# Performance work log

Hardware: AMD Instinct MI355X
Metric: run time of the kernel (lower is better)

## Reference

```python
import jax, jax.numpy as jnp
import numpy as np

B, S, E = 4, 4096, 1024
H, D, L = 16, 64, 64   # heads, head_dim, landmarks
KS = 33                # depthwise conv kernel size (seq dim)
N_ITER = 6


def setup_inputs() -> dict:
    key = jax.random.key(0)
    ks = jax.random.split(key, 8)
    s = 0.02
    return {
        "hidden_states": jax.random.normal(ks[0], (B, S, E), dtype=jnp.float32),
        "Wq": jax.random.normal(ks[1], (E, E), dtype=jnp.float32) * s,
        "bq": jnp.zeros((E,), dtype=jnp.float32),
        "Wk": jax.random.normal(ks[2], (E, E), dtype=jnp.float32) * s,
        "bk": jnp.zeros((E,), dtype=jnp.float32),
        "Wv": jax.random.normal(ks[3], (E, E), dtype=jnp.float32) * s,
        "bv": jnp.zeros((E,), dtype=jnp.float32),
        "conv_w": jax.random.normal(ks[4], (H, 1, KS, 1), dtype=jnp.float32) * 0.1,
    }


def _iterative_pinv_original(a, n_iter=N_ITER):
    # a: [B,H,L,L]. Faithful to _pinv_original_nystrom: GLOBAL max over all batches/heads.
    eye = jnp.eye(a.shape[-1], dtype=a.dtype)
    val = a.swapaxes(-1, -2) / jnp.max(jnp.sum(a, axis=-2))
    for _ in range(n_iter):
        kv = a @ val
        val = 0.25 * val @ (13.0 * eye - kv @ (15.0 * eye - kv @ (7.0 * eye - kv)))
    return val


def reference(hidden_states, Wq, bq, Wk, bk, Wv, bv, conv_w):
    scale = D ** -0.25  # divide q and k each by head_dim**0.25

    def heads(x):  # [B,S,E] -> [B,H,S,D]
        return x.reshape(B, S, H, D).transpose(0, 2, 1, 3)

    q = heads(hidden_states @ Wq + bq) * scale
    k = heads(hidden_states @ Wk + bk) * scale
    v = heads(hidden_states @ Wv + bv)

    # landmark means over segments of length S//L
    ql = q.reshape(B, H, L, S // L, D).mean(axis=-2)  # [B,H,L,D]
    kl = k.reshape(B, H, L, S // L, D).mean(axis=-2)  # [B,H,L,D]

    kernel_1 = jax.nn.softmax(jnp.einsum('bhsd,bhld->bhsl', q, kl), axis=-1)   # [B,H,S,L]
    kernel_2 = jax.nn.softmax(jnp.einsum('bhmd,bhld->bhml', ql, kl), axis=-1)  # [B,H,L,L]
    kernel_3 = jax.nn.softmax(jnp.einsum('bhld,bhsd->bhls', ql, k), axis=-1)   # [B,H,L,S]

    pinv = _iterative_pinv_original(kernel_2)
    attention_probs = kernel_1 @ pinv            # [B,H,S,L]
    new_value = kernel_3 @ v                     # [B,H,L,D]
    ctx = attention_probs @ new_value            # [B,H,S,D]

    # depthwise conv skip on value_layer: Conv2d(H,H,(KS,1),groups=H,bias=False)
    pad = KS // 2
    conv_out = jax.lax.conv_general_dilated(
        v, conv_w, window_strides=(1, 1), padding=((pad, pad), (0, 0)),
        dimension_numbers=('NCHW', 'OIHW', 'NCHW'), feature_group_count=H)
    ctx = ctx + conv_out

    return ctx.transpose(0, 2, 1, 3).reshape(B, S, H * D)
```

## Files before the change

kernel.cpp:

```cpp
#include <hip/hip_runtime.h>
#include <stdint.h>

typedef unsigned short u16;
typedef float f32x4 __attribute__((ext_vector_type(4)));
typedef __bf16 bf16x8 __attribute__((ext_vector_type(8)));
typedef u16 u16x8 __attribute__((ext_vector_type(8)));
typedef u16 u16x4 __attribute__((ext_vector_type(4)));

#define SCALE_QK 0.35355339059327373f

#define BAR() asm volatile("s_barrier" ::: "memory")
#define WAIT_LGKM0() do { asm volatile("s_waitcnt lgkmcnt(0)" ::: "memory"); __builtin_amdgcn_sched_barrier(0); } while (0)
#define WAIT_VM(n) do { asm volatile("s_waitcnt vmcnt(" #n ")" ::: "memory"); __builtin_amdgcn_sched_barrier(0); } while (0)

__device__ __forceinline__ u16 f2bf(float f) {
  union { float f; uint32_t u; } x; x.f = f;
  uint32_t r = x.u + 0x7fffu + ((x.u >> 16) & 1u);
  return (u16)(r >> 16);
}
__device__ __forceinline__ float bf2f(u16 h) {
  union { uint32_t u; float f; } x; x.u = ((uint32_t)h) << 16;
  return x.f;
}
__device__ __forceinline__ void gload16(const void* g, void* l) {
  __builtin_amdgcn_global_load_lds((const __attribute__((address_space(1))) void*)g,
                                   (__attribute__((address_space(3))) void*)l, 16, 0, 0);
}
__device__ __forceinline__ bf16x8 ld_f32_to_bf8(const float* p) {
  f32x4 a = *(const f32x4*)p, b = *(const f32x4*)(p + 4);
  union { u16x8 u; bf16x8 h; } c;
  c.u[0] = f2bf(a[0]); c.u[1] = f2bf(a[1]); c.u[2] = f2bf(a[2]); c.u[3] = f2bf(a[3]);
  c.u[4] = f2bf(b[0]); c.u[5] = f2bf(b[1]); c.u[6] = f2bf(b[2]); c.u[7] = f2bf(b[3]);
  return c.h;
}

__global__ __launch_bounds__(256) void k_prep(const float* __restrict__ hidden,
                                              const float* __restrict__ Wq, const float* __restrict__ Wk,
                                              const float* __restrict__ Wv,
                                              u16* __restrict__ hb, u16* __restrict__ Wt) {
  __shared__ float tile[64][65];
  const int bx = blockIdx.x;
  const int t = threadIdx.x;
  if (bx < 8192) {
    const size_t i = ((size_t)bx * 256 + t) * 8;
    f32x4 v0 = *(const f32x4*)(hidden + i);
    f32x4 v1 = *(const f32x4*)(hidden + i + 4);
    u16x8 o;
    o[0] = f2bf(v0[0]); o[1] = f2bf(v0[1]); o[2] = f2bf(v0[2]); o[3] = f2bf(v0[3]);
    o[4] = f2bf(v1[0]); o[5] = f2bf(v1[1]); o[6] = f2bf(v1[2]); o[7] = f2bf(v1[3]);
    *(u16x8*)(hb + i) = o;
    return;
  }
  const int bxx = bx - 8192;
  const int w = bxx >> 8, tn = (bxx >> 4) & 15, tk = bxx & 15;
  const float* W = (w == 0) ? Wq : ((w == 1) ? Wk : Wv);
  const int r = t >> 2, c0 = (t & 3) * 16;
  const float* src = W + (size_t)(tk * 64 + r) * 1024 + tn * 64 + c0;
#pragma unroll
  for (int j = 0; j < 16; j += 4) {
    f32x4 x = *(const f32x4*)(src + j);
    tile[r][c0 + j + 0] = x[0]; tile[r][c0 + j + 1] = x[1];
    tile[r][c0 + j + 2] = x[2]; tile[r][c0 + j + 3] = x[3];
  }
  __syncthreads();
  u16* dst = Wt + (size_t)(w * 1024 + tn * 64 + r) * 1024 + tk * 64 + c0;
#pragma unroll
  for (int j = 0; j < 16; ++j) dst[j] = f2bf(tile[c0 + j][r]);
}

__device__ __forceinline__ bf16x8 frg(const u16* buf, int row, int ks, int lhi) {
  const int ck = (ks << 2) + lhi;
  return *reinterpret_cast<const bf16x8*>(buf + (row << 6) + ((ck ^ (row & 7)) << 3));
}
__device__ __forceinline__ void issue(const u16* g, int rowbase, int tc, u16* ldsbase, int wid) {
  gload16(g + (((size_t)rowbase) << 10) + tc, ldsbase + ((rowbase + (wid << 3)) << 6));
}
template <int Q>
__device__ __forceinline__ void quad_mfma(const bf16x8 (&af)[2][2], const bf16x8 (&bf)[4][2],
                                          f32x4 (&acc)[8][4]) {
#pragma unroll
  for (int mm = 0; mm < 2; ++mm)
#pragma unroll
    for (int n = 0; n < 4; ++n) {
      acc[Q * 2 + mm][n] = __builtin_amdgcn_mfma_f32_16x16x32_bf16(af[mm][0], bf[n][0], acc[Q * 2 + mm][n], 0, 0, 0);
      acc[Q * 2 + mm][n] = __builtin_amdgcn_mfma_f32_16x16x32_bf16(af[mm][1], bf[n][1], acc[Q * 2 + mm][n], 0, 0, 0);
    }
}
#define LOADA_TO(dst, Q)                                     \
  dst[0][0] = frg(ASr, rA0 + (Q)*32, 0, lhi);                \
  dst[0][1] = frg(ASr, rA0 + (Q)*32, 1, lhi);                \
  dst[1][0] = frg(ASr, rA0 + (Q)*32 + 16, 0, lhi);           \
  dst[1][1] = frg(ASr, rA0 + (Q)*32 + 16, 1, lhi);

__global__ __launch_bounds__(512) void k_gemm2(const u16* __restrict__ A, const u16* __restrict__ Bt,
                                               const float* __restrict__ bq, const float* __restrict__ bk,
                                               const float* __restrict__ bv,
                                               u16* __restrict__ oq, u16* __restrict__ ok, u16* __restrict__ ov,
                                               float* __restrict__ ql, float* __restrict__ kl) {
  __shared__ __align__(16) u16 AS[2][256 * 64];
  __shared__ __align__(16) u16 BS[2][256 * 64];
  __shared__ __align__(16) u16 obuf[8][16][70];
  const int t = threadIdx.x, lane = t & 63, wid = t >> 6;
  const int wm = wid >> 2, wn = wid & 3;
  const int bi = blockIdx.x;
  const int bm = ((bi & 7) << 3) + (bi >> 3) / 12;
  const int bn = (bi >> 3) % 12;
  const int l15 = lane & 15, lhi = lane >> 4;

  const int rowoff = t >> 3;
  const int cswz = (t & 7) ^ (rowoff & 7);
  const u16* aG = A + (((size_t)(bm * 256 + rowoff)) << 10) + (cswz << 3);
  const u16* bG = Bt + (((size_t)(bn * 256 + rowoff)) << 10) + (cswz << 3);

  const int rA0 = wm * 128 + l15;
  const int rB0 = wn * 64 + l15;

  f32x4 acc[8][4];
#pragma unroll
  for (int m = 0; m < 8; ++m)
#pragma unroll
    for (int n = 0; n < 4; ++n) acc[m][n] = (f32x4){0.f, 0.f, 0.f, 0.f};

  issue(bG, 0, 0, BS[0], wid);
  issue(bG, 64, 0, BS[0], wid);
  issue(bG, 128, 0, BS[0], wid);
  issue(bG, 192, 0, BS[0], wid);
  issue(aG, 0, 0, AS[0], wid);
  issue(aG, 128, 0, AS[0], wid);
  issue(aG, 64, 0, AS[0], wid);
  issue(aG, 192, 0, AS[0], wid);
  WAIT_VM(2);
  BAR();

  for (int u = 0; u < 15; ++u) {
    const int pu = u & 1;
    const u16* ASr = AS[pu];
    const u16* BSr = BS[pu];
    u16* ASw = AS[pu ^ 1];
    u16* BSw = BS[pu ^ 1];
    const int tc = (u + 1) << 6;
    bf16x8 bfr[4][2];
    bf16x8 afA[2][2], afB[2][2];
#pragma unroll
    for (int n = 0; n < 4; ++n) {
      bfr[n][0] = frg(BSr, rB0 + n * 16, 0, lhi);
      bfr[n][1] = frg(BSr, rB0 + n * 16, 1, lhi);
    }
    LOADA_TO(afA, 0)
    LOADA_TO(afB, 1)
    issue(bG, 0, tc, BSw, wid);
    issue(bG, 64, tc, BSw, wid);
    issue(bG, 128, tc, BSw, wid);
    issue(bG, 192, tc, BSw, wid);
    issue(aG, 0, tc, ASw, wid);
    issue(aG, 128, tc, ASw, wid);
    issue(aG, 64, tc, ASw, wid);
    issue(aG, 192, tc, ASw, wid);
    __builtin_amdgcn_s_setprio(1);
    quad_mfma<0>(afA, bfr, acc);
    __builtin_amdgcn_s_setprio(0);
    WAIT_VM(8);
    BAR();
    LOADA_TO(afA, 2)
    __builtin_amdgcn_s_setprio(1);
    quad_mfma<1>(afB, bfr, acc);
    __builtin_amdgcn_s_setprio(0);
    LOADA_TO(afB, 3)
    __builtin_amdgcn_s_setprio(1);
    quad_mfma<2>(afA, bfr, acc);
    __builtin_amdgcn_s_setprio(0);
    __builtin_amdgcn_s_setprio(1);
    quad_mfma<3>(afB, bfr, acc);
    __builtin_amdgcn_s_setprio(0);
    WAIT_VM(2);
    BAR();
  }
  {
    const u16* ASr = AS[1];
    const u16* BSr = BS[1];
    bf16x8 bfr[4][2];
    bf16x8 afA[2][2], afB[2][2];
#pragma unroll
    for (int n = 0; n < 4; ++n) {
      bfr[n][0] = frg(BSr, rB0 + n * 16, 0, lhi);
      bfr[n][1] = frg(BSr, rB0 + n * 16, 1, lhi);
    }
    LOADA_TO(afA, 0)
    LOADA_TO(afB, 1)
    quad_mfma<0>(afA, bfr, acc);
    WAIT_VM(0);
    BAR();
    LOADA_TO(afA, 2)
    quad_mfma<1>(afB, bfr, acc);
    LOADA_TO(afB, 3)
    quad_mfma<2>(afA, bfr, acc);
    quad_mfma<3>(afB, bfr, acc);
  }

  const int which = bn >> 2;
  const float* bias = (which == 0) ? bq : ((which == 1) ? bk : bv);
  u16* op = (which == 0) ? oq : ((which == 1) ? ok : ov);
  const float scl = (which < 2) ? SCALE_QK : 1.0f;
  const int h = ((bn & 3) << 2) + wn;
  const int rowBase2 = (bm << 8) + (wm << 7);
  const int rl = lhi << 2;
  const int srow = lane >> 2, d0 = (lane & 3) * 16;
  float bb[4];
#pragma unroll
  for (int n = 0; n < 4; ++n) bb[n] = bias[((bn & 3) << 8) + (wn << 6) + n * 16 + l15];
#pragma unroll
  for (int m = 0; m < 8; ++m) {
#pragma unroll
    for (int n = 0; n < 4; ++n)
#pragma unroll
      for (int r = 0; r < 4; ++r)
        obuf[wid][rl + r][n * 16 + l15] = f2bf((acc[m][n][r] + bb[n]) * scl);
    const int gm = rowBase2 + m * 16 + srow;
    const int b_ = gm >> 12, s = gm & 4095;
    u16* dst = op + (((size_t)b_ * 16 + h) * 4096 + s) * 64 + d0;
    *(u16x8*)dst = *(const u16x8*)&obuf[wid][srow][d0];
    *(u16x8*)(dst + 8) = *(const u16x8*)&obuf[wid][srow][d0 + 8];
  }
  if (which < 2) {
    float* lmp = (which == 0) ? ql : kl;
    const int bh = ((bm >> 4) << 4) + h;
#pragma unroll
    for (int sg = 0; sg < 2; ++sg) {
#pragma unroll
      for (int n = 0; n < 4; ++n) {
        float s = 0.f;
#pragma unroll
        for (int mi = 0; mi < 4; ++mi)
#pragma unroll
          for (int r = 0; r < 4; ++r) s += (acc[sg * 4 + mi][n][r] + bb[n]) * scl;
        s += __shfl_xor(s, 16, 64);
        s += __shfl_xor(s, 32, 64);
        if (lhi == 0) {
          const int lseg = ((bm & 15) << 2) + (wm << 1) + sg;
          lmp[(size_t)bh * 4096 + lseg * 64 + n * 16 + l15] = s * 0.015625f;
        }
      }
    }
  }
}

__global__ __launch_bounds__(256) void k_k2(const float* __restrict__ ql, const float* __restrict__ kl,
                                            float* __restrict__ k2t, float* __restrict__ colmax,
                                            u16* __restrict__ klb) {
  __shared__ __align__(16) float qlT[64 * 68];
  __shared__ __align__(16) float klT[64 * 68];
  __shared__ __align__(16) float sc[64 * 68];
  const int bh = blockIdx.x, t = threadIdx.x;
  {
    const int r = t >> 2, c0 = (t & 3) * 16;
    const float* qp = ql + (size_t)bh * 4096 + r * 64 + c0;
    const float* kp = kl + (size_t)bh * 4096 + r * 64 + c0;
    u16* kb_ = klb + (size_t)bh * 4096 + r * 64 + c0;
#pragma unroll
    for (int j = 0; j < 16; ++j) {
      qlT[(c0 + j) * 68 + r] = qp[j];
      const float kv = kp[j];
      klT[(c0 + j) * 68 + r] = kv;
      kb_[j] = f2bf(kv);
    }
  }
  __syncthreads();
  {
    const int mg = (t >> 4) * 4, lg = (t & 15) * 4;
    float acc[4][4];
#pragma unroll
    for (int i = 0; i < 4; ++i)
#pragma unroll
      for (int j = 0; j < 4; ++j) acc[i][j] = 0.f;
    for (int d0 = 0; d0 < 64; ++d0) {
      f32x4 x = *(const f32x4*)&qlT[d0 * 68 + mg];
      f32x4 y = *(const f32x4*)&klT[d0 * 68 + lg];
#pragma unroll
      for (int i = 0; i < 4; ++i)
#pragma unroll
        for (int j = 0; j < 4; ++j) acc[i][j] += x[i] * y[j];
    }
#pragma unroll
    for (int i = 0; i < 4; ++i)
#pragma unroll
      for (int j = 0; j < 4; ++j) sc[(mg + i) * 68 + lg + j] = acc[i][j];
  }
  __syncthreads();
  if (t < 64) {
    float mx = -1e30f;
    for (int l = 0; l < 64; ++l) mx = fmaxf(mx, sc[t * 68 + l]);
    float sum = 0.f;
    for (int l = 0; l < 64; ++l) { float e = __expf(sc[t * 68 + l] - mx); sc[t * 68 + l] = e; sum += e; }
    const float inv = 1.0f / sum;
    for (int l = 0; l < 64; ++l) sc[t * 68 + l] *= inv;
  }
  __syncthreads();
  {
    const int r = t >> 2, c0 = (t & 3) * 16;
    float* ot = k2t + (size_t)bh * 4096 + r * 64 + c0;
#pragma unroll
    for (int j = 0; j < 16; ++j) ot[j] = sc[(c0 + j) * 68 + r];
  }
  if (t < 64) {
    float s = 0.f;
    for (int m = 0; m < 64; ++m) s += sc[m * 68 + t];
    for (int off = 32; off; off >>= 1) s = fmaxf(s, __shfl_down(s, off, 64));
    if (t == 0) colmax[bh] = s;
  }
}

__device__ __forceinline__ int pidx(int row, int c) {
  return (row << 6) + ((((c >> 2) ^ (row & 15)) << 2) | (c & 3));
}
__device__ __forceinline__ void mm64s(const float* __restrict__ X, const float* __restrict__ Y,
                                      int row, int c0, float* __restrict__ acc) {
#pragma unroll
  for (int j = 0; j < 8; ++j) acc[j] = 0.f;
  for (int kc = 0; kc < 16; ++kc) {
    f32x4 xq = *(const f32x4*)&X[pidx(row, kc << 2)];
#pragma unroll
    for (int kk = 0; kk < 4; ++kk) {
      const int k = (kc << 2) + kk;
      f32x4 y0 = *(const f32x4*)&Y[pidx(k, c0)];
      f32x4 y1 = *(const f32x4*)&Y[pidx(k, c0 + 4)];
      const float x = xq[kk];
#pragma unroll
      for (int j = 0; j < 4; ++j) { acc[j] += x * y0[j]; acc[4 + j] += x * y1[j]; }
    }
  }
}

__global__ __launch_bounds__(512) void k_mid(const float* __restrict__ k2t, const float* __restrict__ colmax,
                                             float* __restrict__ pinv,
                                             const float* __restrict__ ql, const u16* __restrict__ kb,
                                             const u16* __restrict__ vb,
                                             float* __restrict__ nvp, float* __restrict__ zp) {
  __shared__ __align__(16) char smem_s[81920];
  __shared__ float gsh;
  const int t = threadIdx.x;
  if (blockIdx.x < 64) {
    float* aS = (float*)smem_s;
    float* vl = aS + 4096;
    float* kv = vl + 4096;
    float* t1 = kv + 4096;
    float* t2 = t1 + 4096;
    const int bh = blockIdx.x;
    const float* aT = k2t + (size_t)bh * 4096;
    if (t < 64) {
      float v = colmax[t];
      for (int off = 32; off; off >>= 1) v = fmaxf(v, __shfl_down(v, off, 64));
      if (t == 0) gsh = v;
    }
    const int row = t >> 3, c0 = (t & 7) << 3;
#pragma unroll
    for (int j = 0; j < 8; ++j) {
      const int i = t * 8 + j;
      aS[pidx(i & 63, i >> 6)] = aT[i];
    }
    __syncthreads();
    const float ginv = 1.0f / gsh;
    {
      f32x4 v0 = *(const f32x4*)(aT + row * 64 + c0);
      f32x4 v1 = *(const f32x4*)(aT + row * 64 + c0 + 4);
      v0 *= ginv; v1 *= ginv;
      *(f32x4*)&vl[pidx(row, c0)] = v0;
      *(f32x4*)&vl[pidx(row, c0 + 4)] = v1;
    }
    __syncthreads();
    float acc[8];
    for (int it = 0; it < 6; ++it) {
      mm64s(aS, vl, row, c0, acc);
#pragma unroll
      for (int j = 0; j < 8; ++j) kv[pidx(row, c0 + j)] = acc[j];
      __syncthreads();
#pragma unroll
      for (int j = 0; j < 8; ++j) {
        const int c = c0 + j;
        t1[pidx(row, c)] = ((row == c) ? 7.0f : 0.0f) - kv[pidx(row, c)];
      }
      __syncthreads();
      mm64s(kv, t1, row, c0, acc);
#pragma unroll
      for (int j = 0; j < 8; ++j) {
        const int c = c0 + j;
        t2[pidx(row, c)] = ((row == c) ? 15.0f : 0.0f) - acc[j];
      }
      __syncthreads();
      mm64s(kv, t2, row, c0, acc);
#pragma unroll
      for (int j = 0; j < 8; ++j) {
        const int c = c0 + j;
        t1[pidx(row, c)] = ((row == c) ? 13.0f : 0.0f) - acc[j];
      }
      __syncthreads();
      mm64s(vl, t1, row, c0, acc);
#pragma unroll
      for (int j = 0; j < 8; ++j) t2[pidx(row, c0 + j)] = 0.25f * acc[j];
      __syncthreads();
#pragma unroll
      for (int j = 0; j < 8; ++j) vl[pidx(row, c0 + j)] = t2[pidx(row, c0 + j)];
      __syncthreads();
    }
    {
      f32x4 o0 = *(const f32x4*)&vl[pidx(row, c0)];
      f32x4 o1 = *(const f32x4*)&vl[pidx(row, c0 + 4)];
      *(f32x4*)(pinv + (size_t)bh * 4096 + row * 64 + c0) = o0;
      *(f32x4*)(pinv + (size_t)bh * 4096 + row * 64 + c0 + 4) = o1;
    }
    return;
  }
  u16* VTs = (u16*)smem_s;
  u16* els = (u16*)(smem_s + 36864);
  const int id = (int)blockIdx.x - 64;
  const int bh = id & 63, scn = id >> 6;
  const int lane = t & 63, w = t >> 6;
  const int wq = w & 3, half = w >> 2;
  const int l15 = lane & 15, kg = (lane >> 4) << 3, rl = (lane >> 4) << 2;
  const float* aRow = ql + (size_t)bh * 4096 + (wq * 16 + l15) * 64 + kg;
  bf16x8 aql[2];
  aql[0] = ld_f32_to_bf8(aRow);
  aql[1] = ld_f32_to_bf8(aRow + 32);
  f32x4 accv[4];
#pragma unroll
  for (int n = 0; n < 4; ++n) accv[n] = (f32x4){0.f, 0.f, 0.f, 0.f};
  float zacc[4] = {0.f, 0.f, 0.f, 0.f};
  const int sBase = scn * 512 + half * 256;
  u16* VT0 = VTs + ((size_t)(0 * 2 + half) * 64) * 72;
  u16* VT1 = VTs + ((size_t)(1 * 2 + half) * 64) * 72;
  u16* elw = els + ((size_t)w * 16) * 72;
  {
    const u16* vp = vb + ((size_t)bh * 4096 + sBase + lane) * 64 + wq * 16;
    u16x8 h0 = *(const u16x8*)vp, h1 = *(const u16x8*)(vp + 8);
#pragma unroll
    for (int j = 0; j < 8; ++j) {
      VT0[(wq * 16 + j) * 72 + lane] = h0[j];
      VT0[(wq * 16 + 8 + j) * 72 + lane] = h1[j];
    }
  }
  __syncthreads();
  for (int sub = 0; sub < 4; ++sub) {
    const int s0 = sBase + sub * 64;
    u16x8 hn0 = {0, 0, 0, 0, 0, 0, 0, 0}, hn1 = {0, 0, 0, 0, 0, 0, 0, 0};
    if (sub < 3) {
      const u16* vpn = vb + ((size_t)bh * 4096 + s0 + 64 + lane) * 64 + wq * 16;
      hn0 = *(const u16x8*)vpn; hn1 = *(const u16x8*)(vpn + 8);
    }
    const u16* bRow = kb + ((size_t)bh * 4096 + s0 + l15) * 64 + kg;
    f32x4 e[4];
#pragma unroll
    for (int n = 0; n < 4; ++n) e[n] = (f32x4){0.f, 0.f, 0.f, 0.f};
#pragma unroll
    for (int ks = 0; ks < 2; ++ks)
#pragma unroll
      for (int n = 0; n < 4; ++n) {
        bf16x8 bk_ = *reinterpret_cast<const bf16x8*>(bRow + n * 1024 + ks * 32);
        e[n] = __builtin_amdgcn_mfma_f32_16x16x32_bf16(aql[ks], bk_, e[n], 0, 0, 0);
      }
#pragma unroll
    for (int n = 0; n < 4; ++n)
#pragma unroll
      for (int r = 0; r < 4; ++r) {
        const float v = __expf(e[n][r]);
        zacc[r] += v;
        elw[(rl + r) * 72 + n * 16 + l15] = f2bf(v);
      }
    if (sub < 3) {
      u16* VTn = ((sub + 1) & 1) ? VT1 : VT0;
#pragma unroll
      for (int j = 0; j < 8; ++j) {
        VTn[(wq * 16 + j) * 72 + lane] = hn0[j];
        VTn[(wq * 16 + 8 + j) * 72 + lane] = hn1[j];
      }
    }
    WAIT_LGKM0();
    const u16* VTc = (sub & 1) ? VT1 : VT0;
#pragma unroll
    for (int ks = 0; ks < 2; ++ks) {
      bf16x8 af = *reinterpret_cast<const bf16x8*>(&elw[l15 * 72 + kg + ks * 32]);
#pragma unroll
      for (int n = 0; n < 4; ++n) {
        bf16x8 bf_ = *reinterpret_cast<const bf16x8*>(&VTc[(n * 16 + l15) * 72 + kg + ks * 32]);
        accv[n] = __builtin_amdgcn_mfma_f32_16x16x32_bf16(af, bf_, accv[n], 0, 0, 0);
      }
    }
    BAR();
  }
  const int p = scn * 2 + half;
#pragma unroll
  for (int r = 0; r < 4; ++r)
#pragma unroll
    for (int n = 0; n < 4; ++n)
      nvp[(((size_t)p * 64 + bh) * 64 + wq * 16 + rl + r) * 64 + n * 16 + l15] = accv[n][r];
#pragma unroll
  for (int r = 0; r < 4; ++r) {
    float s = zacc[r];
    s += __shfl_xor(s, 1, 64); s += __shfl_xor(s, 2, 64);
    s += __shfl_xor(s, 4, 64); s += __shfl_xor(s, 8, 64);
    if (l15 == 0) zp[((size_t)p * 64 + bh) * 64 + wq * 16 + rl + r] = s;
  }
}

__global__ __launch_bounds__(256) void k_pnv(const float* __restrict__ pinv, const float* __restrict__ nvp,
                                             const float* __restrict__ zp, u16* __restrict__ Mtb) {
  __shared__ __align__(16) float XT[64 * 68];
  __shared__ __align__(16) float Y[64 * 68];
  const int bh = blockIdx.x, t = threadIdx.x;
  {
    const int r = t >> 2, c0 = (t & 3) * 16;
    const float* pp = pinv + (size_t)bh * 4096 + r * 64 + c0;
#pragma unroll
    for (int j = 0; j < 16; ++j) XT[(c0 + j) * 68 + r] = pp[j];
    float zs = 0.f;
#pragma unroll
    for (int p = 0; p < 16; ++p) zs += zp[((size_t)p * 64 + bh) * 64 + r];
    const float iz = 1.0f / zs;
#pragma unroll
    for (int j = 0; j < 16; ++j) {
      float s = 0.f;
#pragma unroll
      for (int p = 0; p < 16; ++p) s += nvp[(((size_t)p * 64 + bh) * 64 + r) * 64 + c0 + j];
      Y[r * 68 + c0 + j] = s * iz;
    }
  }
  __syncthreads();
  const int rg = (t >> 4) * 4, cg = (t & 15) * 4;
  float acc[4][4];
#pragma unroll
  for (int i = 0; i < 4; ++i)
#pragma unroll
    for (int j = 0; j < 4; ++j) acc[i][j] = 0.f;
  for (int k = 0; k < 64; ++k) {
    f32x4 x = *(const f32x4*)&XT[k * 68 + rg];
    f32x4 y = *(const f32x4*)&Y[k * 68 + cg];
#pragma unroll
    for (int i = 0; i < 4; ++i)
#pragma unroll
      for (int j = 0; j < 4; ++j) acc[i][j] += x[i] * y[j];
  }
#pragma unroll
  for (int j = 0; j < 4; ++j) {
    u16x4 o = {f2bf(acc[0][j]), f2bf(acc[1][j]), f2bf(acc[2][j]), f2bf(acc[3][j])};
    *(u16x4*)&Mtb[(size_t)bh * 4096 + (cg + j) * 64 + rg] = o;
  }
}

__global__ __launch_bounds__(256) void k_out(const u16* __restrict__ qb, const u16* __restrict__ vb,
                                             const u16* __restrict__ klb, const u16* __restrict__ Mtb,
                                             const float* __restrict__ cw, float* __restrict__ out) {
  __shared__ __align__(16) u16 P_lds[4][16][72];
  __shared__ __align__(16) u16 vtile_t[64][100];
  __shared__ float wsh[33];
  const int bid = blockIdx.x;
  const int bh = bid >> 6, st = bid & 63;
  const int b = bh >> 4, h = bh & 15;
  const int t = threadIdx.x, lane = t & 63, w = t >> 6;
  const int sbase = st * 64;
  const int l15 = lane & 15, kg = (lane >> 4) << 3, rl = (lane >> 4) << 2;

  if (t < 33) wsh[t] = cw[h * 33 + t];
  for (int idx = t; idx < 96 * 8; idx += 256) {
    const int row = idx >> 3, c8 = idx & 7;
    const int sg = sbase + row - 16;
    u16x8 val = {0, 0, 0, 0, 0, 0, 0, 0};
    if (sg >= 0 && sg < 4096) val = *(const u16x8*)(vb + ((size_t)bh * 4096 + sg) * 64 + c8 * 8);
#pragma unroll
    for (int j = 0; j < 8; ++j) vtile_t[c8 * 8 + j][row] = val[j];
  }

  f32x4 c1[4];
#pragma unroll
  for (int n = 0; n < 4; ++n) c1[n] = (f32x4){0.f, 0.f, 0.f, 0.f};
  {
    const u16* aRow = qb + ((size_t)bh * 4096 + sbase + w * 16 + l15) * 64 + kg;
    const u16* kRow = klb + (size_t)bh * 4096 + l15 * 64 + kg;
#pragma unroll
    for (int ks = 0; ks < 2; ++ks) {
      bf16x8 af = *reinterpret_cast<const bf16x8*>(aRow + ks * 32);
#pragma unroll
      for (int n = 0; n < 4; ++n) {
        bf16x8 bf_ = *reinterpret_cast<const bf16x8*>(kRow + n * 1024 + ks * 32);
        c1[n] = __builtin_amdgcn_mfma_f32_16x16x32_bf16(af, bf_, c1[n], 0, 0, 0);
      }
    }
  }
  float invZ[4];
  {
    float z[4] = {0.f, 0.f, 0.f, 0.f};
#pragma unroll
    for (int n = 0; n < 4; ++n)
#pragma unroll
      for (int r = 0; r < 4; ++r) { float v = __expf(c1[n][r]); c1[n][r] = v; z[r] += v; }
#pragma unroll
    for (int r = 0; r < 4; ++r) {
      float s = z[r];
      s += __shfl_xor(s, 1, 64); s += __shfl_xor(s, 2, 64);
      s += __shfl_xor(s, 4, 64); s += __shfl_xor(s, 8, 64);
      invZ[r] = 1.0f / s;
    }
#pragma unroll
    for (int n = 0; n < 4; ++n)
#pragma unroll
      for (int r = 0; r < 4; ++r)
        P_lds[w][rl + r][n * 16 + l15] = f2bf(c1[n][r]);
  }
  __syncthreads();
  f32x4 c2[4];
#pragma unroll
  for (int n = 0; n < 4; ++n) c2[n] = (f32x4){0.f, 0.f, 0.f, 0.f};
  {
    const u16* mRow = Mtb + (size_t)bh * 4096 + l15 * 64 + kg;
#pragma unroll
    for (int ks = 0; ks < 2; ++ks) {
      bf16x8 af = *reinterpret_cast<const bf16x8*>(&P_lds[w][l15][kg + ks * 32]);
#pragma unroll
      for (int n = 0; n < 4; ++n) {
        bf16x8 bf_ = *reinterpret_cast<const bf16x8*>(mRow + n * 1024 + ks * 32);
        c2[n] = __builtin_amdgcn_mfma_f32_16x16x32_bf16(af, bf_, c2[n], 0, 0, 0);
      }
    }
  }
  const int base = w * 16 + rl;
#pragma unroll
  for (int n = 0; n < 4; ++n) {
    const int d = n * 16 + l15;
    float vcol[36];
#pragma unroll
    for (int k8 = 0; k8 < 9; ++k8) {
      u16x4 vq = *(const u16x4*)&vtile_t[d][base + k8 * 4];
      vcol[k8 * 4 + 0] = bf2f(vq[0]); vcol[k8 * 4 + 1] = bf2f(vq[1]);
      vcol[k8 * 4 + 2] = bf2f(vq[2]); vcol[k8 * 4 + 3] = bf2f(vq[3]);
    }
    float cv[4] = {0.f, 0.f, 0.f, 0.f};
#pragma unroll
    for (int jt = 0; jt < 33; ++jt) {
      const float ww = wsh[jt];
#pragma unroll
      for (int r = 0; r < 4; ++r) cv[r] += ww * vcol[r + jt];
    }
#pragma unroll
    for (int r = 0; r < 4; ++r) {
      const int sgl = sbase + base + r;
      out[((size_t)b * 4096 + sgl) * 1024 + h * 64 + d] = c2[n][r] * invZ[r] + cv[r];
    }
  }
}

extern "C" void kernel_launch(void* const* d_in, const int* in_sizes, int n_in,
                              void* d_out, int out_size, void* d_ws, size_t ws_size,
                              hipStream_t stream) {
  const float* hidden = (const float*)d_in[0];
  const float* Wq = (const float*)d_in[1];
  const float* bq = (const float*)d_in[2];
  const float* Wk = (const float*)d_in[3];
  const float* bk = (const float*)d_in[4];
  const float* Wv = (const float*)d_in[5];
  const float* bv = (const float*)d_in[6];
  const float* cw = (const float*)d_in[7];
  float* out = (float*)d_out;

  char* ws = (char*)d_ws;
  u16* qb = (u16*)(ws);
  u16* kb = (u16*)(ws + 33554432ull);
  u16* vb = (u16*)(ws + 67108864ull);
  float* ql = (float*)(ws + 100663296ull);
  float* kl = (float*)(ws + 101711872ull);
  float* k2t = (float*)(ws + 102760448ull);
  float* pinvb = (float*)(ws + 103809024ull);
  u16* Mtb = (u16*)(ws + 104857600ull);
  u16* klb = (u16*)(ws + 105381888ull);
  float* stats = (float*)(ws + 106430464ull);
  u16* wt = (u16*)(ws + 106434560ull);
  u16* hb = (u16*)(ws + 112726016ull);
  float* nvp = (float*)(ws + 112726016ull);
  float* zp = (float*)(ws + 129503232ull);

  k_prep<<<8960, 256, 0, stream>>>(hidden, Wq, Wk, Wv, hb, wt);
  k_gemm2<<<768, 512, 0, stream>>>(hb, wt, bq, bk, bv, qb, kb, vb, ql, kl);
  k_k2<<<64, 256, 0, stream>>>(ql, kl, k2t, stats, klb);
  k_mid<<<576, 512, 0, stream>>>(k2t, stats, pinvb, ql, kb, vb, nvp, zp);
  k_pnv<<<64, 256, 0, stream>>>(pinvb, nvp, zp, Mtb);
  k_out<<<4096, 256, 0, stream>>>(qb, vb, klb, Mtb, cw, out);
  (void)in_sizes; (void)n_in; (void)out_size; (void)ws_size;
}
```

Before: 318.9 us.

## Reschedule GEMM loads, drop block swizzle, split mid kernel into pinv and s3nv

The QKV GEMM main loop now uses a single A-fragment register set with extra barriers and LDS waits interleaved between the four MFMA quarters. The grouped block-index swizzle is replaced by a plain 2D grid, which loses the L2 locality it provided. The fused k_mid kernel, which ran the pinv and kernel3@V work in separate blocks of one launch, is split into two launches: k_pinv, and k_s3nv with 256-thread blocks each covering 512 sequence positions, so k_pnv reduces 8 partials instead of 16. These look like regressions: extra barriers, worse L2 tiling, and the pinv no longer overlapping the s3nv work.

New measurement: 339.6 us. +6.5%, slower.

```diff
diff --git a/kernel.cpp b/kernel.cpp
--- a/kernel.cpp
+++ b/kernel.cpp
@@ -86,11 +86,11 @@
       acc[Q * 2 + mm][n] = __builtin_amdgcn_mfma_f32_16x16x32_bf16(af[mm][1], bf[n][1], acc[Q * 2 + mm][n], 0, 0, 0);
     }
 }
-#define LOADA_TO(dst, Q)                                     \
-  dst[0][0] = frg(ASr, rA0 + (Q)*32, 0, lhi);                \
-  dst[0][1] = frg(ASr, rA0 + (Q)*32, 1, lhi);                \
-  dst[1][0] = frg(ASr, rA0 + (Q)*32 + 16, 0, lhi);           \
-  dst[1][1] = frg(ASr, rA0 + (Q)*32 + 16, 1, lhi);
+#define LOADA(Q)                                             \
+  af[0][0] = frg(ASr, rA0 + (Q)*32, 0, lhi);                 \
+  af[0][1] = frg(ASr, rA0 + (Q)*32, 1, lhi);                 \
+  af[1][0] = frg(ASr, rA0 + (Q)*32 + 16, 0, lhi);            \
+  af[1][1] = frg(ASr, rA0 + (Q)*32 + 16, 1, lhi);
 
 __global__ __launch_bounds__(512) void k_gemm2(const u16* __restrict__ A, const u16* __restrict__ Bt,
                                                const float* __restrict__ bq, const float* __restrict__ bk,
@@ -102,9 +102,7 @@
   __shared__ __align__(16) u16 obuf[8][16][70];
   const int t = threadIdx.x, lane = t & 63, wid = t >> 6;
   const int wm = wid >> 2, wn = wid & 3;
-  const int bi = blockIdx.x;
-  const int bm = ((bi & 7) << 3) + (bi >> 3) / 12;
-  const int bn = (bi >> 3) % 12;
+  const int bm = blockIdx.x, bn = blockIdx.y;
   const int l15 = lane & 15, lhi = lane >> 4;
 
   const int rowoff = t >> 3;
@@ -140,37 +138,47 @@
     u16* BSw = BS[pu ^ 1];
     const int tc = (u + 1) << 6;
     bf16x8 bfr[4][2];
-    bf16x8 afA[2][2], afB[2][2];
+    bf16x8 af[2][2];
 #pragma unroll
     for (int n = 0; n < 4; ++n) {
       bfr[n][0] = frg(BSr, rB0 + n * 16, 0, lhi);
       bfr[n][1] = frg(BSr, rB0 + n * 16, 1, lhi);
     }
-    LOADA_TO(afA, 0)
-    LOADA_TO(afB, 1)
+    LOADA(0)
     issue(bG, 0, tc, BSw, wid);
     issue(bG, 64, tc, BSw, wid);
     issue(bG, 128, tc, BSw, wid);
     issue(bG, 192, tc, BSw, wid);
+    BAR();
+    WAIT_LGKM0();
+    __builtin_amdgcn_s_setprio(1);
+    quad_mfma<0>(af, bfr, acc);
+    __builtin_amdgcn_s_setprio(0);
+    BAR();
+    LOADA(1)
     issue(aG, 0, tc, ASw, wid);
     issue(aG, 128, tc, ASw, wid);
+    BAR();
+    WAIT_LGKM0();
+    __builtin_amdgcn_s_setprio(1);
+    quad_mfma<1>(af, bfr, acc);
+    __builtin_amdgcn_s_setprio(0);
+    WAIT_VM(6);
+    BAR();
+    LOADA(2)
     issue(aG, 64, tc, ASw, wid);
     issue(aG, 192, tc, ASw, wid);
+    BAR();
+    WAIT_LGKM0();
     __builtin_amdgcn_s_setprio(1);
-    quad_mfma<0>(afA, bfr, acc);
+    quad_mfma<2>(af, bfr, acc);
     __builtin_amdgcn_s_setprio(0);
-    WAIT_VM(8);
-    BAR();
-    LOADA_TO(afA, 2)
+    BAR();
+    LOADA(3)
+    BAR();
+    WAIT_LGKM0();
     __builtin_amdgcn_s_setprio(1);
-    quad_mfma<1>(afB, bfr, acc);
-    __builtin_amdgcn_s_setprio(0);
-    LOADA_TO(afB, 3)
-    __builtin_amdgcn_s_setprio(1);
-    quad_mfma<2>(afA, bfr, acc);
-    __builtin_amdgcn_s_setprio(0);
-    __builtin_amdgcn_s_setprio(1);
-    quad_mfma<3>(afB, bfr, acc);
+    quad_mfma<3>(af, bfr, acc);
     __builtin_amdgcn_s_setprio(0);
     WAIT_VM(2);
     BAR();
@@ -179,22 +187,22 @@
     const u16* ASr = AS[1];
     const u16* BSr = BS[1];
     bf16x8 bfr[4][2];
-    bf16x8 afA[2][2], afB[2][2];
+    bf16x8 af[2][2];
 #pragma unroll
     for (int n = 0; n < 4; ++n) {
       bfr[n][0] = frg(BSr, rB0 + n * 16, 0, lhi);
       bfr[n][1] = frg(BSr, rB0 + n * 16, 1, lhi);
     }
-    LOADA_TO(afA, 0)
-    LOADA_TO(afB, 1)
-    quad_mfma<0>(afA, bfr, acc);
+    LOADA(0)
+    quad_mfma<0>(af, bfr, acc);
+    LOADA(1)
+    quad_mfma<1>(af, bfr, acc);
     WAIT_VM(0);
     BAR();
-    LOADA_TO(afA, 2)
-    quad_mfma<1>(afB, bfr, acc);
-    LOADA_TO(afB, 3)
-    quad_mfma<2>(afA, bfr, acc);
-    quad_mfma<3>(afB, bfr, acc);
+    LOADA(2)
+    quad_mfma<2>(af, bfr, acc);
+    LOADA(3)
+    quad_mfma<3>(af, bfr, acc);
   }
 
   const int which = bn >> 2;
@@ -330,93 +338,88 @@
   }
 }
 
-__global__ __launch_bounds__(512) void k_mid(const float* __restrict__ k2t, const float* __restrict__ colmax,
-                                             float* __restrict__ pinv,
-                                             const float* __restrict__ ql, const u16* __restrict__ kb,
-                                             const u16* __restrict__ vb,
-                                             float* __restrict__ nvp, float* __restrict__ zp) {
-  __shared__ __align__(16) char smem_s[81920];
+__global__ __launch_bounds__(512) void k_pinv(const float* __restrict__ k2t, const float* __restrict__ colmax,
+                                              float* __restrict__ pinv) {
+  __shared__ __align__(16) float aS[4096];
+  __shared__ __align__(16) float vl[4096];
+  __shared__ __align__(16) float kv[4096];
+  __shared__ __align__(16) float t1[4096];
+  __shared__ __align__(16) float t2[4096];
   __shared__ float gsh;
-  const int t = threadIdx.x;
-  if (blockIdx.x < 64) {
-    float* aS = (float*)smem_s;
-    float* vl = aS + 4096;
-    float* kv = vl + 4096;
-    float* t1 = kv + 4096;
-    float* t2 = t1 + 4096;
-    const int bh = blockIdx.x;
-    const float* aT = k2t + (size_t)bh * 4096;
-    if (t < 64) {
-      float v = colmax[t];
-      for (int off = 32; off; off >>= 1) v = fmaxf(v, __shfl_down(v, off, 64));
-      if (t == 0) gsh = v;
-    }
-    const int row = t >> 3, c0 = (t & 7) << 3;
+  const int bh = blockIdx.x, t = threadIdx.x;
+  const float* aT = k2t + (size_t)bh * 4096;
+  if (t < 64) {
+    float v = colmax[t];
+    for (int off = 32; off; off >>= 1) v = fmaxf(v, __shfl_down(v, off, 64));
+    if (t == 0) gsh = v;
+  }
+  const int row = t >> 3, c0 = (t & 7) << 3;
+#pragma unroll
+  for (int j = 0; j < 8; ++j) {
+    const int i = t * 8 + j;
+    aS[pidx(i & 63, i >> 6)] = aT[i];
+  }
+  __syncthreads();
+  const float ginv = 1.0f / gsh;
+  {
+    f32x4 v0 = *(const f32x4*)(aT + row * 64 + c0);
+    f32x4 v1 = *(const f32x4*)(aT + row * 64 + c0 + 4);
+    v0 *= ginv; v1 *= ginv;
+    *(f32x4*)&vl[pidx(row, c0)] = v0;
+    *(f32x4*)&vl[pidx(row, c0 + 4)] = v1;
+  }
+  __syncthreads();
+  float acc[8];
+  for (int it = 0; it < 6; ++it) {
+    mm64s(aS, vl, row, c0, acc);
+#pragma unroll
+    for (int j = 0; j < 8; ++j) kv[pidx(row, c0 + j)] = acc[j];
+    __syncthreads();
 #pragma unroll
     for (int j = 0; j < 8; ++j) {
-      const int i = t * 8 + j;
-      aS[pidx(i & 63, i >> 6)] = aT[i];
+      const int c = c0 + j;
+      t1[pidx(row, c)] = ((row == c) ? 7.0f : 0.0f) - kv[pidx(row, c)];
     }
     __syncthreads();
-    const float ginv = 1.0f / gsh;
-    {
-      f32x4 v0 = *(const f32x4*)(aT + row * 64 + c0);
-      f32x4 v1 = *(const f32x4*)(aT + row * 64 + c0 + 4);
-      v0 *= ginv; v1 *= ginv;
-      *(f32x4*)&vl[pidx(row, c0)] = v0;
-      *(f32x4*)&vl[pidx(row, c0 + 4)] = v1;
+    mm64s(kv, t1, row, c0, acc);
+#pragma unroll
+    for (int j = 0; j < 8; ++j) {
+      const int c = c0 + j;
+      t2[pidx(row, c)] = ((row == c) ? 15.0f : 0.0f) - acc[j];
     }
     __syncthreads();
-    float acc[8];
-    for (int it = 0; it < 6; ++it) {
-      mm64s(aS, vl, row, c0, acc);
-#pragma unroll
-      for (int j = 0; j < 8; ++j) kv[pidx(row, c0 + j)] = acc[j];
-      __syncthreads();
-#pragma unroll
-      for (int j = 0; j < 8; ++j) {
-        const int c = c0 + j;
-        t1[pidx(row, c)] = ((row == c) ? 7.0f : 0.0f) - kv[pidx(row, c)];
-      }
-      __syncthreads();
-      mm64s(kv, t1, row, c0, acc);
-#pragma unroll
-      for (int j = 0; j < 8; ++j) {
-        const int c = c0 + j;
-        t2[pidx(row, c)] = ((row == c) ? 15.0f : 0.0f) - acc[j];
-      }
-      __syncthreads();
-      mm64s(kv, t2, row, c0, acc);
-#pragma unroll
-      for (int j = 0; j < 8; ++j) {
-        const int c = c0 + j;
-        t1[pidx(row, c)] = ((row == c) ? 13.0f : 0.0f) - acc[j];
-      }
-      __syncthreads();
-      mm64s(vl, t1, row, c0, acc);
-#pragma unroll
-      for (int j = 0; j < 8; ++j) t2[pidx(row, c0 + j)] = 0.25f * acc[j];
-      __syncthreads();
-#pragma unroll
-      for (int j = 0; j < 8; ++j) vl[pidx(row, c0 + j)] = t2[pidx(row, c0 + j)];
-      __syncthreads();
-    }
-    {
-      f32x4 o0 = *(const f32x4*)&vl[pidx(row, c0)];
-      f32x4 o1 = *(const f32x4*)&vl[pidx(row, c0 + 4)];
-      *(f32x4*)(pinv + (size_t)bh * 4096 + row * 64 + c0) = o0;
-      *(f32x4*)(pinv + (size_t)bh * 4096 + row * 64 + c0 + 4) = o1;
-    }
-    return;
-  }
-  u16* VTs = (u16*)smem_s;
-  u16* els = (u16*)(smem_s + 36864);
-  const int id = (int)blockIdx.x - 64;
-  const int bh = id & 63, scn = id >> 6;
-  const int lane = t & 63, w = t >> 6;
-  const int wq = w & 3, half = w >> 2;
+    mm64s(kv, t2, row, c0, acc);
+#pragma unroll
+    for (int j = 0; j < 8; ++j) {
+      const int c = c0 + j;
+      t1[pidx(row, c)] = ((row == c) ? 13.0f : 0.0f) - acc[j];
+    }
+    __syncthreads();
+    mm64s(vl, t1, row, c0, acc);
+#pragma unroll
+    for (int j = 0; j < 8; ++j) t2[pidx(row, c0 + j)] = 0.25f * acc[j];
+    __syncthreads();
+#pragma unroll
+    for (int j = 0; j < 8; ++j) vl[pidx(row, c0 + j)] = t2[pidx(row, c0 + j)];
+    __syncthreads();
+  }
+  {
+    f32x4 o0 = *(const f32x4*)&vl[pidx(row, c0)];
+    f32x4 o1 = *(const f32x4*)&vl[pidx(row, c0 + 4)];
+    *(f32x4*)(pinv + (size_t)bh * 4096 + row * 64 + c0) = o0;
+    *(f32x4*)(pinv + (size_t)bh * 4096 + row * 64 + c0 + 4) = o1;
+  }
+}
+
+__global__ __launch_bounds__(256) void k_s3nv(const float* __restrict__ ql, const u16* __restrict__ kb,
+                                              const u16* __restrict__ vb,
+                                              float* __restrict__ nvp, float* __restrict__ zp) {
+  __shared__ __align__(16) u16 VT[2][64][72];
+  __shared__ __align__(16) u16 e_lds[4][16][72];
+  const int bh = blockIdx.x, scn = blockIdx.y;
+  const int t = threadIdx.x, lane = t & 63, w = t >> 6;
   const int l15 = lane & 15, kg = (lane >> 4) << 3, rl = (lane >> 4) << 2;
-  const float* aRow = ql + (size_t)bh * 4096 + (wq * 16 + l15) * 64 + kg;
+  const float* aRow = ql + (size_t)bh * 4096 + (w * 16 + l15) * 64 + kg;
   bf16x8 aql[2];
   aql[0] = ld_f32_to_bf8(aRow);
   aql[1] = ld_f32_to_bf8(aRow + 32);
@@ -424,25 +427,19 @@
 #pragma unroll
   for (int n = 0; n < 4; ++n) accv[n] = (f32x4){0.f, 0.f, 0.f, 0.f};
   float zacc[4] = {0.f, 0.f, 0.f, 0.f};
-  const int sBase = scn * 512 + half * 256;
-  u16* VT0 = VTs + ((size_t)(0 * 2 + half) * 64) * 72;
-  u16* VT1 = VTs + ((size_t)(1 * 2 + half) * 64) * 72;
-  u16* elw = els + ((size_t)w * 16) * 72;
-  {
-    const u16* vp = vb + ((size_t)bh * 4096 + sBase + lane) * 64 + wq * 16;
+  const int sBase = scn * 512;
+  {
+    const u16* vp = vb + ((size_t)bh * 4096 + sBase + lane) * 64 + w * 16;
     u16x8 h0 = *(const u16x8*)vp, h1 = *(const u16x8*)(vp + 8);
 #pragma unroll
-    for (int j = 0; j < 8; ++j) {
-      VT0[(wq * 16 + j) * 72 + lane] = h0[j];
-      VT0[(wq * 16 + 8 + j) * 72 + lane] = h1[j];
-    }
-  }
-  __syncthreads();
-  for (int sub = 0; sub < 4; ++sub) {
+    for (int j = 0; j < 8; ++j) { VT[0][w * 16 + j][lane] = h0[j]; VT[0][w * 16 + 8 + j][lane] = h1[j]; }
+  }
+  __syncthreads();
+  for (int sub = 0; sub < 8; ++sub) {
     const int s0 = sBase + sub * 64;
     u16x8 hn0 = {0, 0, 0, 0, 0, 0, 0, 0}, hn1 = {0, 0, 0, 0, 0, 0, 0, 0};
-    if (sub < 3) {
-      const u16* vpn = vb + ((size_t)bh * 4096 + s0 + 64 + lane) * 64 + wq * 16;
+    if (sub < 7) {
+      const u16* vpn = vb + ((size_t)bh * 4096 + s0 + 64 + lane) * 64 + w * 16;
       hn0 = *(const u16x8*)vpn; hn1 = *(const u16x8*)(vpn + 8);
     }
     const u16* bRow = kb + ((size_t)bh * 4096 + s0 + l15) * 64 + kg;
@@ -462,41 +459,37 @@
       for (int r = 0; r < 4; ++r) {
         const float v = __expf(e[n][r]);
         zacc[r] += v;
-        elw[(rl + r) * 72 + n * 16 + l15] = f2bf(v);
+        e_lds[w][rl + r][n * 16 + l15] = f2bf(v);
       }
-    if (sub < 3) {
-      u16* VTn = ((sub + 1) & 1) ? VT1 : VT0;
-#pragma unroll
-      for (int j = 0; j < 8; ++j) {
-        VTn[(wq * 16 + j) * 72 + lane] = hn0[j];
-        VTn[(wq * 16 + 8 + j) * 72 + lane] = hn1[j];
-      }
+    if (sub < 7) {
+      const int nb = (sub + 1) & 1;
+#pragma unroll
+      for (int j = 0; j < 8; ++j) { VT[nb][w * 16 + j][lane] = hn0[j]; VT[nb][w * 16 + 8 + j][lane] = hn1[j]; }
     }
     WAIT_LGKM0();
-    const u16* VTc = (sub & 1) ? VT1 : VT0;
+    const int cb = sub & 1;
 #pragma unroll
     for (int ks = 0; ks < 2; ++ks) {
-      bf16x8 af = *reinterpret_cast<const bf16x8*>(&elw[l15 * 72 + kg + ks * 32]);
+      bf16x8 af = *reinterpret_cast<const bf16x8*>(&e_lds[w][l15][kg + ks * 32]);
 #pragma unroll
       for (int n = 0; n < 4; ++n) {
-        bf16x8 bf_ = *reinterpret_cast<const bf16x8*>(&VTc[(n * 16 + l15) * 72 + kg + ks * 32]);
+        bf16x8 bf_ = *reinterpret_cast<const bf16x8*>(&VT[cb][n * 16 + l15][kg + ks * 32]);
         accv[n] = __builtin_amdgcn_mfma_f32_16x16x32_bf16(af, bf_, accv[n], 0, 0, 0);
       }
     }
     BAR();
   }
-  const int p = scn * 2 + half;
 #pragma unroll
   for (int r = 0; r < 4; ++r)
 #pragma unroll
     for (int n = 0; n < 4; ++n)
-      nvp[(((size_t)p * 64 + bh) * 64 + wq * 16 + rl + r) * 64 + n * 16 + l15] = accv[n][r];
+      nvp[(((size_t)scn * 64 + bh) * 64 + w * 16 + rl + r) * 64 + n * 16 + l15] = accv[n][r];
 #pragma unroll
   for (int r = 0; r < 4; ++r) {
     float s = zacc[r];
     s += __shfl_xor(s, 1, 64); s += __shfl_xor(s, 2, 64);
     s += __shfl_xor(s, 4, 64); s += __shfl_xor(s, 8, 64);
-    if (l15 == 0) zp[((size_t)p * 64 + bh) * 64 + wq * 16 + rl + r] = s;
+    if (l15 == 0) zp[((size_t)scn * 64 + bh) * 64 + w * 16 + rl + r] = s;
   }
 }
 
@@ -512,13 +505,13 @@
     for (int j = 0; j < 16; ++j) XT[(c0 + j) * 68 + r] = pp[j];
     float zs = 0.f;
 #pragma unroll
-    for (int p = 0; p < 16; ++p) zs += zp[((size_t)p * 64 + bh) * 64 + r];
+    for (int p = 0; p < 8; ++p) zs += zp[((size_t)p * 64 + bh) * 64 + r];
     const float iz = 1.0f / zs;
 #pragma unroll
     for (int j = 0; j < 16; ++j) {
       float s = 0.f;
 #pragma unroll
-      for (int p = 0; p < 16; ++p) s += nvp[(((size_t)p * 64 + bh) * 64 + r) * 64 + c0 + j];
+      for (int p = 0; p < 8; ++p) s += nvp[(((size_t)p * 64 + bh) * 64 + r) * 64 + c0 + j];
       Y[r * 68 + c0 + j] = s * iz;
     }
   }
@@ -672,12 +665,13 @@
   u16* wt = (u16*)(ws + 106434560ull);
   u16* hb = (u16*)(ws + 112726016ull);
   float* nvp = (float*)(ws + 112726016ull);
-  float* zp = (float*)(ws + 129503232ull);
+  float* zp = (float*)(ws + 121114624ull);
 
   k_prep<<<8960, 256, 0, stream>>>(hidden, Wq, Wk, Wv, hb, wt);
-  k_gemm2<<<768, 512, 0, stream>>>(hb, wt, bq, bk, bv, qb, kb, vb, ql, kl);
+  k_gemm2<<<dim3(64, 12), 512, 0, stream>>>(hb, wt, bq, bk, bv, qb, kb, vb, ql, kl);
   k_k2<<<64, 256, 0, stream>>>(ql, kl, k2t, stats, klb);
-  k_mid<<<576, 512, 0, stream>>>(k2t, stats, pinvb, ql, kb, vb, nvp, zp);
+  k_pinv<<<64, 512, 0, stream>>>(k2t, stats, pinvb);
+  k_s3nv<<<dim3(64, 8), 256, 0, stream>>>(ql, kb, vb, nvp, zp);
   k_pnv<<<64, 256, 0, stream>>>(pinvb, nvp, zp, Mtb);
   k_out<<<4096, 256, 0, stream>>>(qb, vb, klb, Mtb, cw, out);
   (void)in_sizes; (void)n_in; (void)out_size; (void)ws_size;
```
